# Optimization experiments

Hardware: AMD Instinct MI355X
Metric: run time of the kernel (lower is better)

## Reference

```python
import jax, jax.numpy as jnp
import numpy as np

RPE_LEN = 14  # rpe_length
HEADS = 10
HDIM = 64
EMBED = 640
DFF = 2560


def layer_norm(x, g, b, eps=1e-5):
    mu = jnp.mean(x, axis=-1, keepdims=True)
    var = jnp.var(x, axis=-1, keepdims=True)
    return (x - mu) * jax.lax.rsqrt(var + eps) * g + b


def rpe_embeddings(table_v, table_h, N):
    """RelativePosition2D.forward(N, N) -> [N, N, head_dim]."""
    L = N - 1
    s = int(L ** 0.5)  # 14 for N=197
    r = jnp.arange(L)
    dist_v = r[None, :] // s - r[:, None] // s
    dist_h = r[None, :] % s - r[:, None] % s
    idx_v = jnp.clip(dist_v, -RPE_LEN, RPE_LEN) + RPE_LEN + 1
    idx_h = jnp.clip(dist_h, -RPE_LEN, RPE_LEN) + RPE_LEN + 1
    # pad one row/col of zeros at the front (class token -> index 0)
    idx_v = jnp.pad(idx_v, ((1, 0), (1, 0)))
    idx_h = jnp.pad(idx_h, ((1, 0), (1, 0)))
    return table_v[idx_v] + table_h[idx_h]


def setup_inputs() -> dict:
    key = jax.random.key(0)
    ks = jax.random.split(key, 20)
    B, N, E, H, D, F = 64, 197, EMBED, HEADS, HDIM, DFF
    T = 2 * RPE_LEN + 2  # 30
    std = 0.02
    return {
        "x": jax.random.normal(ks[0], (B, N, E), jnp.float32),
        "ln1_g": jnp.ones((E,), jnp.float32),
        "ln1_b": jnp.zeros((E,), jnp.float32),
        "Wq": jax.random.normal(ks[1], (H * D, E), jnp.float32) * std,
        "Wk": jax.random.normal(ks[2], (H * D, E), jnp.float32) * std,
        "Wv": jax.random.normal(ks[3], (H * D, E), jnp.float32) * std,
        "Wp": jax.random.normal(ks[4], (E, H * D), jnp.float32) * std,
        "bp": jnp.zeros((E,), jnp.float32),
        "rpk_v": jax.random.normal(ks[5], (T, D), jnp.float32) * std,
        "rpk_h": jax.random.normal(ks[6], (T, D), jnp.float32) * std,
        "rpv_v": jax.random.normal(ks[7], (T, D), jnp.float32) * std,
        "rpv_h": jax.random.normal(ks[8], (T, D), jnp.float32) * std,
        "ln2_g": jnp.ones((E,), jnp.float32),
        "ln2_b": jnp.zeros((E,), jnp.float32),
        "W1": jax.random.normal(ks[9], (F, E), jnp.float32) * std,
        "b1": jnp.zeros((F,), jnp.float32),
        "W2": jax.random.normal(ks[10], (E, F), jnp.float32) * std,
        "b2": jnp.zeros((E,), jnp.float32),
    }


def reference(x, ln1_g, ln1_b, Wq, Wk, Wv, Wp, bp,
              rpk_v, rpk_h, rpv_v, rpv_h,
              ln2_g, ln2_b, W1, b1, W2, b2):
    B, N, E = x.shape
    H, D = HEADS, HDIM
    scale = D ** (-0.5)

    # --- attention block (pre-norm) ---
    residual = x
    h = layer_norm(x, ln1_g, ln1_b)
    q = (h @ Wq.T).reshape(B, N, H, D)
    k = (h @ Wk.T).reshape(B, N, H, D)
    v = (h @ Wv.T).reshape(B, N, H, D)

    attn = jnp.einsum('bnhd,bmhd->bhnm', q, k) * scale
    r_p_k = rpe_embeddings(rpk_v, rpk_h, N)          # [N, N, D]
    attn = attn + jnp.einsum('bnhd,nmd->bhnm', q, r_p_k) * scale
    attn = jax.nn.softmax(attn, axis=-1)

    o = jnp.einsum('bhnm,bmhd->bhnd', attn, v)
    r_p_v = rpe_embeddings(rpv_v, rpv_h, N)          # [N, N, D]
    o = o + jnp.einsum('bhnm,nmd->bhnd', attn, r_p_v)
    o = o.transpose(0, 2, 1, 3).reshape(B, N, H * D)
    x = residual + o @ Wp.T + bp

    # --- FFN block (pre-norm) ---
    residual = x
    h = layer_norm(x, ln2_g, ln2_b)
    h = jax.nn.gelu(h @ W1.T + b1, approximate=False)
    x = residual + h @ W2.T + b2
    return x
```

## Files before the change

### kernel.cpp

```cpp
#include <hip/hip_runtime.h>
#include <hip/hip_bf16.h>
#include <math.h>

#define NN   197
#define EE   640
#define HH   10
#define DD   64
#define FF   2560
#define MTOK (64 * 197)
#define RPE_T 30
#define NCONV 17

typedef __hip_bfloat16 bf16;
typedef __attribute__((ext_vector_type(8))) __bf16 bf16x8;
typedef __attribute__((ext_vector_type(4))) float  floatx4;
typedef __attribute__((ext_vector_type(8))) unsigned short ushort8;

#define MFMA32(a, b, c) __builtin_amdgcn_mfma_f32_16x16x32_bf16(a, b, c, 0, 0, 0)

__device__ __forceinline__ float bfbits2f(unsigned short u) {
    union { unsigned int i; float f; } x; x.i = ((unsigned int)u) << 16; return x.f;
}
__device__ __forceinline__ unsigned short f2bf(float f) {
    bf16 t = __float2bfloat16(f);
    unsigned short u; __builtin_memcpy(&u, &t, 2); return u;
}
__device__ __forceinline__ void gld16(const bf16* g, bf16* l) {
    __builtin_amdgcn_global_load_lds(
        (const __attribute__((address_space(1))) unsigned int*)g,
        (__attribute__((address_space(3))) unsigned int*)l, 16, 0, 0);
}
__device__ __forceinline__ float gelu_f(float v) {
    float y = 0.7978845608f * (v + 0.044715f * v * v * v);
    float a = fabsf(y);
    float e = __expf(-2.f * a);
    float t = (1.f - e) / (1.f + e);
    t = (y < 0.f) ? -t : t;
    return 0.5f * v * (1.f + t);
}

__global__ void detect_kernel(const unsigned int* __restrict__ g, int* __restrict__ flag) {
    if (threadIdx.x == 0) flag[0] = (g[0] == 0x3F800000u) ? 1 : 0;
}

struct ConvDesc {
    const void* src[NCONV];
    bf16*       dst[NCONV];
    int         end8[NCONV];
};

__global__ __launch_bounds__(256) void conv_fused(
    ConvDesc d, int total8, const int* __restrict__ flag)
{
    int c = blockIdx.x * 256 + threadIdx.x;
    if (c >= total8) return;
    int s = 0, start = 0;
#pragma unroll
    for (int i = 0; i < NCONV - 1; ++i) {
        if (c >= d.end8[i]) { s = i + 1; start = d.end8[i]; }
    }
    int local = c - start;
    if (flag[0]) {
        const float* sp = (const float*)d.src[s] + (size_t)local * 8;
        bf16 t[8];
#pragma unroll
        for (int j = 0; j < 8; ++j) t[j] = __float2bfloat16(sp[j]);
        *(ushort8*)(d.dst[s] + (size_t)local * 8) = *(const ushort8*)t;
    } else {
        ((ushort8*)d.dst[s])[local] = ((const ushort8*)d.src[s])[local];
    }
}

__global__ __launch_bounds__(256) void rpetrans_kernel(
    const bf16* __restrict__ rvv, const bf16* __restrict__ rvh,
    unsigned short* __restrict__ rvvT, unsigned short* __restrict__ rvhT)
{
    int t = blockIdx.x * 256 + threadIdx.x;
    if (t < 64 * 32) {
        int d = t >> 5, tt = t & 31;
        rvvT[t] = (tt < RPE_T) ? ((const unsigned short*)rvv)[tt * 64 + d] : 0;
        rvhT[t] = (tt < RPE_T) ? ((const unsigned short*)rvh)[tt * 64 + d] : 0;
    }
}

__global__ __launch_bounds__(256) void selbuild_kernel(
    bf16* __restrict__ SelV, bf16* __restrict__ SelH)
{
    int t = blockIdx.x * 256 + threadIdx.x;
    if (t < 16 * 224) {
        int j = t / 224, m = t % 224;
        bool valid = (j < 14) && (m >= 1) && (m < 197);
        SelV[t] = __float2bfloat16((valid && (m - 1) / 14 == j) ? 1.f : 0.f);
        SelH[t] = __float2bfloat16((valid && (m - 1) % 14 == j) ? 1.f : 0.f);
    }
}

__global__ __launch_bounds__(256) void vtrans_kernel(
    const bf16* __restrict__ qkv, unsigned short* __restrict__ VtG)
{
    int bh = blockIdx.x;
    int b = bh / HH, h = bh % HH;
    unsigned short* dst = VtG + (size_t)bh * (64 * 224);
    for (int t = threadIdx.x; t < 224 * 8; t += 256) {
        int m = t >> 3, d8 = (t & 7) << 3;
        ushort8 val = {0, 0, 0, 0, 0, 0, 0, 0};
        if (m < NN)
            val = *(const ushort8*)(qkv + ((size_t)b * NN + m) * 1920 + 1280 + h * 64 + d8);
#pragma unroll
        for (int j = 0; j < 8; ++j) dst[(d8 + j) * 224 + m] = val[j];
    }
}

__global__ __launch_bounds__(256) void ln_kernel(
    const void* __restrict__ xb, size_t xrow0, int xdyn,
    const int* __restrict__ flag,
    const bf16* __restrict__ g, const bf16* __restrict__ b,
    bf16* __restrict__ out, int nrows)
{
    int row  = blockIdx.x * 4 + (threadIdx.x >> 6);
    if (row >= nrows) return;
    int lane = threadIdx.x & 63;
    const int f32 = xdyn && flag[0];
    const size_t base = (xrow0 + row) * (size_t)EE;
    float vals[10];
    float s = 0.f, ss = 0.f;
#pragma unroll
    for (int j = 0; j < 10; ++j) {
        int e = j * 64 + lane;
        float f = f32 ? ((const float*)xb)[base + e]
                      : (float)((const bf16*)xb)[base + e];
        vals[j] = f; s += f; ss += f * f;
    }
#pragma unroll
    for (int off = 32; off; off >>= 1) {
        s  += __shfl_xor(s, off);
        ss += __shfl_xor(ss, off);
    }
    float mean = s * (1.f / EE);
    float var  = ss * (1.f / EE) - mean * mean;
    float rs   = rsqrtf(var + 1e-5f);
#pragma unroll
    for (int j = 0; j < 10; ++j) {
        int e = j * 64 + lane;
        float hv = (vals[j] - mean) * rs * (float)g[e] + (float)b[e];
        out[(size_t)row * EE + e] = __float2bfloat16(hv);
    }
}

template <int KK, int GELU>
__global__ __launch_bounds__(256) void gemm128(
    const bf16* __restrict__ A, const bf16* __restrict__ B,
    const bf16* __restrict__ bias,
    const void* __restrict__ residb, size_t resid_row0, int resid_dyn,
    void* __restrict__ outb, size_t out_row0, int out_dyn,
    const int* __restrict__ flag,
    int M, int N)
{
    __shared__ bf16 At[2][128 * 32];
    __shared__ bf16 Bt[2][128 * 32];

    const int tid  = threadIdx.x;
    const int wave = tid >> 6, lane = tid & 63;
    const int quad = lane >> 4, l16 = lane & 15;
    const int wy = wave >> 1, wx = wave & 1;
    const int n0 = blockIdx.x * 128;
    const int m0 = blockIdx.y * 128;

    const int drow   = wave * 16 + (lane >> 2);
    const int gchunk = ((lane & 3) ^ ((lane >> 3) & 3)) * 8;
    const int ar0 = min(m0 + drow, M - 1);
    const int ar1 = min(m0 + 64 + drow, M - 1);
    const bf16* Ag0 = A + (size_t)ar0 * KK + gchunk;
    const bf16* Ag1 = A + (size_t)ar1 * KK + gchunk;
    const bf16* Bg0 = B + (size_t)(n0 + drow) * KK + gchunk;
    const bf16* Bg1 = B + (size_t)(n0 + 64 + drow) * KK + gchunk;
    const int lo0 = wave * 512;
    const int lo1 = 2048 + wave * 512;

    const int swz = (quad ^ ((l16 >> 1) & 3)) * 8;

    floatx4 acc[4][4] = {};
    constexpr int NK = KK / 64;

    auto body = [&](int k0) {
        __syncthreads();
        gld16(Ag0 + k0,      &At[0][lo0]);
        gld16(Ag1 + k0,      &At[0][lo1]);
        gld16(Ag0 + k0 + 32, &At[1][lo0]);
        gld16(Ag1 + k0 + 32, &At[1][lo1]);
        gld16(Bg0 + k0,      &Bt[0][lo0]);
        gld16(Bg1 + k0,      &Bt[0][lo1]);
        gld16(Bg0 + k0 + 32, &Bt[1][lo0]);
        gld16(Bg1 + k0 + 32, &Bt[1][lo1]);
        __syncthreads();
#pragma unroll
        for (int kk = 0; kk < 2; ++kk) {
            bf16x8 af[4], bfr[4];
#pragma unroll
            for (int s = 0; s < 4; ++s)
                af[s] = *(const bf16x8*)(&At[kk][(wy * 64 + s * 16 + l16) * 32 + swz]);
#pragma unroll
            for (int t = 0; t < 4; ++t)
                bfr[t] = *(const bf16x8*)(&Bt[kk][(wx * 64 + t * 16 + l16) * 32 + swz]);
#pragma unroll
            for (int s = 0; s < 4; ++s)
#pragma unroll
                for (int t = 0; t < 4; ++t)
                    acc[s][t] = MFMA32(af[s], bfr[t], acc[s][t]);
        }
    };

    if constexpr (NK <= 16) {
#pragma unroll
        for (int k = 0; k < NK; ++k) body(k * 64);
    } else {
#pragma unroll 4
        for (int k = 0; k < NK; ++k) body(k * 64);
    }

    const int fr = resid_dyn && flag[0];
    const int fo = out_dyn && flag[0];
    float bv[4];
#pragma unroll
    for (int t = 0; t < 4; ++t)
        bv[t] = bias ? (float)bias[n0 + wx * 64 + t * 16 + l16] : 0.f;

#pragma unroll
    for (int s = 0; s < 4; ++s) {
#pragma unroll
        for (int i = 0; i < 4; ++i) {
            int m = m0 + wy * 64 + s * 16 + quad * 4 + i;
            if (m < M) {
                size_t rowoff_o = (out_row0 + m) * (size_t)N;
                size_t rowoff_r = (resid_row0 + m) * (size_t)N;
#pragma unroll
                for (int t = 0; t < 4; ++t) {
                    int n = n0 + wx * 64 + t * 16 + l16;
                    float v = acc[s][t][i] + bv[t];
                    if (GELU) v = gelu_f(v);
                    if (residb)
                        v += fr ? ((const float*)residb)[rowoff_r + n]
                                : (float)((const bf16*)residb)[rowoff_r + n];
                    if (fo) ((float*)outb)[rowoff_o + n] = v;
                    else    ((bf16*)outb)[rowoff_o + n]  = __float2bfloat16(v);
                }
            }
        }
    }
}

__global__ __launch_bounds__(256) void attn_kernel(
    const bf16* __restrict__ qkv,
    const bf16* __restrict__ tkv, const bf16* __restrict__ tkh,
    const unsigned short* __restrict__ rvvT,
    const unsigned short* __restrict__ rvhT,
    const unsigned short* __restrict__ VtG,
    const bf16* __restrict__ SelV, const bf16* __restrict__ SelH,
    bf16* __restrict__ o)
{
    __shared__ unsigned short Pm[64 * 232];
    __shared__ unsigned short PSv[64 * 40];
    __shared__ unsigned short PSh[64 * 40];
    __shared__ unsigned short QTv[64 * 32];
    __shared__ unsigned short QTh[64 * 32];

    const int tid  = threadIdx.x;
    const int wave = tid >> 6, lane = tid & 63;
    const int quad = lane >> 4, l16 = lane & 15;
    const int b  = blockIdx.x / HH, h = blockIdx.x % HH;
    const int qt = blockIdx.y;
    const size_t rowbase = (size_t)b * NN;

    for (int t = tid; t < 64 * 40; t += 256) { PSv[t] = 0; PSh[t] = 0; }
    for (int t = tid; t < 64 * 24; t += 256) Pm[(t / 24) * 232 + 208 + (t % 24)] = 0;
    __syncthreads();

    const int rA = qt * 64 + wave * 16 + l16;
    const bf16* qrow = qkv + (rowbase + min(rA, NN - 1)) * 1920 + h * 64;
    bf16x8 qa0 = *(const bf16x8*)(qrow + quad * 8);
    bf16x8 qa1 = *(const bf16x8*)(qrow + 32 + quad * 8);

    {
        floatx4 av[2] = {}, ah[2] = {};
#pragma unroll
        for (int ct = 0; ct < 2; ++ct) {
            int t = min(ct * 16 + l16, RPE_T - 1);
            av[ct] = MFMA32(qa0, *(const bf16x8*)(tkv + t * 64 + quad * 8), av[ct]);
            av[ct] = MFMA32(qa1, *(const bf16x8*)(tkv + t * 64 + 32 + quad * 8), av[ct]);
            ah[ct] = MFMA32(qa0, *(const bf16x8*)(tkh + t * 64 + quad * 8), ah[ct]);
            ah[ct] = MFMA32(qa1, *(const bf16x8*)(tkh + t * 64 + 32 + quad * 8), ah[ct]);
        }
#pragma unroll
        for (int ct = 0; ct < 2; ++ct)
#pragma unroll
            for (int i = 0; i < 4; ++i) {
                int row = wave * 16 + quad * 4 + i;
                QTv[row * 32 + ct * 16 + l16] = f2bf(av[ct][i]);
                QTh[row * 32 + ct * 16 + l16] = f2bf(ah[ct][i]);
            }
    }

    floatx4 sacc[13];
#pragma unroll
    for (int mt = 0; mt < 13; ++mt) {
        const bf16* krow = qkv + (rowbase + min(mt * 16 + l16, NN - 1)) * 1920
                           + 640 + h * 64;
        floatx4 a = {};
        a = MFMA32(qa0, *(const bf16x8*)(krow + quad * 8), a);
        a = MFMA32(qa1, *(const bf16x8*)(krow + 32 + quad * 8), a);
        sacc[mt] = a;
    }

    int nn4[4], jn4[4], in4[4];
#pragma unroll
    for (int i = 0; i < 4; ++i) {
        int n = qt * 64 + wave * 16 + quad * 4 + i;
        nn4[i] = n;
        jn4[i] = (n > 0) ? (n - 1) / 14 : 0;
        in4[i] = (n > 0) ? (n - 1) % 14 : 0;
    }
    float mx4[4] = {-3e38f, -3e38f, -3e38f, -3e38f};
#pragma unroll
    for (int mt = 0; mt < 13; ++mt) {
        int m = mt * 16 + l16;
        int jm = (m > 0) ? (m - 1) / 14 : 0;
        int im = (m > 0) ? (m - 1) % 14 : 0;
        bool mok = (m < NN);
#pragma unroll
        for (int i = 0; i < 4; ++i) {
            int row = wave * 16 + quad * 4 + i;
            int iv = (nn4[i] == 0 || m == 0) ? 0 : (jm - jn4[i] + 15);
            int ih = (nn4[i] == 0 || m == 0) ? 0 : (im - in4[i] + 15);
            float val = mok ? (sacc[mt][i] + bfbits2f(QTv[row * 32 + iv])
                               + bfbits2f(QTh[row * 32 + ih])) * 0.125f
                            : -3e38f;
            sacc[mt][i] = val;
            mx4[i] = fmaxf(mx4[i], val);
        }
    }
#pragma unroll
    for (int i = 0; i < 4; ++i)
#pragma unroll
        for (int off = 1; off < 16; off <<= 1)
            mx4[i] = fmaxf(mx4[i], __shfl_xor(mx4[i], off));

    float sm4[4] = {0.f, 0.f, 0.f, 0.f};
#pragma unroll
    for (int mt = 0; mt < 13; ++mt) {
#pragma unroll
        for (int i = 0; i < 4; ++i) {
            float p = __expf(sacc[mt][i] - mx4[i]);
            sm4[i] += p;
            Pm[(wave * 16 + quad * 4 + i) * 232 + mt * 16 + l16] = f2bf(p);
        }
    }
#pragma unroll
    for (int i = 0; i < 4; ++i)
#pragma unroll
        for (int off = 1; off < 16; off <<= 1)
            sm4[i] += __shfl_xor(sm4[i], off);

    floatx4 oacc[4] = {};
    floatx4 psv = {}, psh = {};
    const unsigned short* vt = VtG + (size_t)blockIdx.x * (64 * 224);
    for (int k0 = 0; k0 < 224; k0 += 32) {
        bf16x8 pa = *(const bf16x8*)(const void*)&Pm[(wave * 16 + l16) * 232 + k0 + quad * 8];
#pragma unroll
        for (int ct = 0; ct < 4; ++ct) {
            bf16x8 vb = *(const bf16x8*)(const void*)&vt[(ct * 16 + l16) * 224 + k0 + quad * 8];
            oacc[ct] = MFMA32(pa, vb, oacc[ct]);
        }
        psv = MFMA32(pa, *(const bf16x8*)(SelV + l16 * 224 + k0 + quad * 8), psv);
        psh = MFMA32(pa, *(const bf16x8*)(SelH + l16 * 224 + k0 + quad * 8), psh);
    }

#pragma unroll
    for (int i = 0; i < 4; ++i) {
        int row = wave * 16 + quad * 4 + i;
        int n = qt * 64 + row;
        if (n >= 1 && n < NN && l16 < 14) {
            int jn2 = (n - 1) / 14, in2 = (n - 1) % 14;
            PSv[row * 40 + (l16 - jn2 + 15)] = f2bf(psv[i]);
            PSh[row * 40 + (l16 - in2 + 15)] = f2bf(psh[i]);
        }
    }
    if (lane < 16) {
        int row = wave * 16 + lane;
        int n = qt * 64 + row;
        if (n < NN) {
            float p0 = (n == 0) ? sm4[0] : bfbits2f(Pm[row * 232]);
            PSv[row * 40] = f2bf(p0);
            PSh[row * 40] = f2bf(p0);
        }
    }

    {
        bf16x8 pav = *(const bf16x8*)(const void*)&PSv[(wave * 16 + l16) * 40 + quad * 8];
        bf16x8 pah = *(const bf16x8*)(const void*)&PSh[(wave * 16 + l16) * 40 + quad * 8];
#pragma unroll
        for (int ct = 0; ct < 4; ++ct) {
            bf16x8 bv  = *(const bf16x8*)(const void*)&rvvT[(ct * 16 + l16) * 32 + quad * 8];
            bf16x8 bh2 = *(const bf16x8*)(const void*)&rvhT[(ct * 16 + l16) * 32 + quad * 8];
            oacc[ct] = MFMA32(pav, bv,  oacc[ct]);
            oacc[ct] = MFMA32(pah, bh2, oacc[ct]);
        }
    }
#pragma unroll
    for (int i = 0; i < 4; ++i) {
        float rinv = 1.f / sm4[i];
        int row = wave * 16 + quad * 4 + i;
        int n = qt * 64 + row;
        if (n < NN) {
#pragma unroll
            for (int ct = 0; ct < 4; ++ct)
                o[(rowbase + n) * 640 + h * 64 + ct * 16 + l16] =
                    __float2bfloat16(oacc[ct][i] * rinv);
        }
    }
}

extern "C" void kernel_launch(void* const* d_in, const int* in_sizes, int n_in,
                              void* d_out, int out_size, void* d_ws, size_t ws_size,
                              hipStream_t stream)
{
    const void* xraw = d_in[0];
    char* ws = (char*)d_ws;
    size_t off = 0;
    auto alloc = [&](size_t bytes) -> void* {
        void* p = ws + off;
        off += (bytes + 255) & ~(size_t)255;
        return p;
    };

    int* flag = (int*)alloc(256);
    bf16* Wqc  = (bf16*)alloc((size_t)EE * EE * 2);
    bf16* Wkc  = (bf16*)alloc((size_t)EE * EE * 2);
    bf16* Wvc  = (bf16*)alloc((size_t)EE * EE * 2);
    bf16* Wpc  = (bf16*)alloc((size_t)EE * EE * 2);
    bf16* W1c  = (bf16*)alloc((size_t)FF * EE * 2);
    bf16* W2c  = (bf16*)alloc((size_t)EE * FF * 2);
    bf16* l1g  = (bf16*)alloc(EE * 2);
    bf16* l1b  = (bf16*)alloc(EE * 2);
    bf16* l2g  = (bf16*)alloc(EE * 2);
    bf16* l2b  = (bf16*)alloc(EE * 2);
    bf16* bpc  = (bf16*)alloc(EE * 2);
    bf16* b1c  = (bf16*)alloc(FF * 2);
    bf16* b2c  = (bf16*)alloc(EE * 2);
    bf16* rkv  = (bf16*)alloc(RPE_T * DD * 2);
    bf16* rkh  = (bf16*)alloc(RPE_T * DD * 2);
    bf16* rvv  = (bf16*)alloc(RPE_T * DD * 2);
    bf16* rvh  = (bf16*)alloc(RPE_T * DD * 2);
    unsigned short* rvvT = (unsigned short*)alloc(64 * 32 * 2);
    unsigned short* rvhT = (unsigned short*)alloc(64 * 32 * 2);
    bf16* SelV = (bf16*)alloc(16 * 224 * 2);
    bf16* SelH = (bf16*)alloc(16 * 224 * 2);
    const size_t cvt_end = off;

    int Bc = 0;
    const int cands[6] = {64, 32, 16, 8, 4, 2};
    for (int i = 0; i < 6; ++i) {
        size_t rows = (size_t)NN * cands[i];
        size_t need = cvt_end + rows * 10240 + (size_t)cands[i] * HH * 64 * 224 * 2 + 8192;
        if (need <= ws_size) { Bc = cands[i]; break; }
    }
    if (Bc == 0) return;

    const int nchunks = 64 / Bc;
    const int rows    = NN * Bc;
    bf16* h1   = (bf16*)alloc((size_t)rows * EE * 2);
    bf16* qkvb = (bf16*)alloc((size_t)rows * 1920 * 2);
    bf16* h3   = (bf16*)alloc((size_t)rows * FF * 2);
    unsigned short* VtG = (unsigned short*)alloc((size_t)Bc * HH * 64 * 224 * 2);

    detect_kernel<<<1, 64, 0, stream>>>((const unsigned int*)d_in[1], flag);
    {
        ConvDesc cd;
        const void* srcs[NCONV] = { d_in[3], d_in[4], d_in[5], d_in[6],
                                    d_in[14], d_in[16], d_in[1], d_in[2], d_in[12],
                                    d_in[13], d_in[7], d_in[15], d_in[17], d_in[8],
                                    d_in[9], d_in[10], d_in[11] };
        bf16* dsts[NCONV] = { Wqc, Wkc, Wvc, Wpc, W1c, W2c, l1g, l1b, l2g,
                              l2b, bpc, b1c, b2c, rkv, rkh, rvv, rvh };
        int ns[NCONV] = { EE * EE, EE * EE, EE * EE, EE * EE, FF * EE,
                          EE * FF, EE, EE, EE, EE, EE, FF, EE,
                          RPE_T * DD, RPE_T * DD, RPE_T * DD, RPE_T * DD };
        int cum = 0;
        for (int i = 0; i < NCONV; ++i) {
            cd.src[i] = srcs[i]; cd.dst[i] = dsts[i];
            cum += ns[i] / 8; cd.end8[i] = cum;
        }
        conv_fused<<<(cum + 255) / 256, 256, 0, stream>>>(cd, cum, flag);
    }
    rpetrans_kernel<<<8, 256, 0, stream>>>(rvv, rvh, rvvT, rvhT);
    selbuild_kernel<<<14, 256, 0, stream>>>(SelV, SelH);

    const int gM128 = (rows + 127) / 128;
    const int gLN   = (rows + 3) / 4;

    for (int c = 0; c < nchunks; ++c) {
        const size_t row0 = (size_t)c * rows;

        ln_kernel<<<gLN, 256, 0, stream>>>(xraw, row0, 1, flag, l1g, l1b, h1, rows);

        gemm128<EE, 0><<<dim3(1920 / 128, gM128), 256, 0, stream>>>(
            h1, Wqc, nullptr, nullptr, 0, 0, qkvb, 0, 0, flag, rows, 1920);

        vtrans_kernel<<<Bc * HH, 256, 0, stream>>>(qkvb, VtG);

        attn_kernel<<<dim3(Bc * HH, 4), 256, 0, stream>>>(
            qkvb, rkv, rkh, rvvT, rvhT, VtG, SelV, SelH, h1);

        gemm128<EE, 0><<<dim3(EE / 128, gM128), 256, 0, stream>>>(
            h1, Wpc, bpc, xraw, row0, 1, d_out, row0, 1, flag, rows, EE);
    }

    for (int c = 0; c < nchunks; ++c) {
        const size_t row0 = (size_t)c * rows;

        ln_kernel<<<gLN, 256, 0, stream>>>(d_out, row0, 1, flag, l2g, l2b, h1, rows);

        gemm128<EE, 1><<<dim3(FF / 128, gM128), 256, 0, stream>>>(
            h1, W1c, b1c, nullptr, 0, 0, h3, 0, 0, flag, rows, FF);

        gemm128<FF, 0><<<dim3(EE / 128, gM128), 256, 0, stream>>>(
            h3, W2c, b2c, d_out, row0, 1, d_out, row0, 1, flag, rows, EE);
    }
}
```

Before: 479.2 us.

## Pre-swizzle K, V, RPE tables and selectors into MFMA fragment order

Adds a pre-pass that rewrites K, V, the RPE key/value tables and the selector matrices into a lane-contiguous MFMA operand layout. The attention kernel can then fetch each B fragment as one contiguous 16-byte load per lane instead of strided row gathers. K is now copied as well as V, which adds extra global traffic in the transpose kernel, and the V transpose does scalar strided reads. The intent is better coalescing in the attention inner loops.

```diff
diff --git a/kernel.cpp b/kernel.cpp
--- a/kernel.cpp
+++ b/kernel.cpp
@@ -71,43 +71,61 @@
     }
 }
 
-__global__ __launch_bounds__(256) void rpetrans_kernel(
+__global__ __launch_bounds__(256) void tabflat_kernel(
+    const bf16* __restrict__ tkv, const bf16* __restrict__ tkh,
     const bf16* __restrict__ rvv, const bf16* __restrict__ rvh,
-    unsigned short* __restrict__ rvvT, unsigned short* __restrict__ rvhT)
-{
-    int t = blockIdx.x * 256 + threadIdx.x;
-    if (t < 64 * 32) {
-        int d = t >> 5, tt = t & 31;
-        rvvT[t] = (tt < RPE_T) ? ((const unsigned short*)rvv)[tt * 64 + d] : 0;
-        rvhT[t] = (tt < RPE_T) ? ((const unsigned short*)rvh)[tt * 64 + d] : 0;
-    }
-}
-
-__global__ __launch_bounds__(256) void selbuild_kernel(
-    bf16* __restrict__ SelV, bf16* __restrict__ SelH)
-{
-    int t = blockIdx.x * 256 + threadIdx.x;
-    if (t < 16 * 224) {
-        int j = t / 224, m = t % 224;
-        bool valid = (j < 14) && (m >= 1) && (m < 197);
-        SelV[t] = __float2bfloat16((valid && (m - 1) / 14 == j) ? 1.f : 0.f);
-        SelH[t] = __float2bfloat16((valid && (m - 1) % 14 == j) ? 1.f : 0.f);
-    }
-}
-
-__global__ __launch_bounds__(256) void vtrans_kernel(
-    const bf16* __restrict__ qkv, unsigned short* __restrict__ VtG)
+    unsigned short* __restrict__ tkvL, unsigned short* __restrict__ tkhL,
+    unsigned short* __restrict__ rvvL, unsigned short* __restrict__ rvhL,
+    bf16* __restrict__ SelVL, bf16* __restrict__ SelHL)
+{
+    int i = blockIdx.x * 256 + threadIdx.x;
+    int f = i >> 9, r = i & 511, quad = r >> 7, l16 = (r >> 3) & 15, j = i & 7;
+    if (i < 2048) {
+        int ct = f >> 1, kk = f & 1, t = ct * 16 + l16, d = kk * 32 + quad * 8 + j;
+        tkvL[i] = (t < RPE_T) ? ((const unsigned short*)tkv)[t * 64 + d] : 0;
+        tkhL[i] = (t < RPE_T) ? ((const unsigned short*)tkh)[t * 64 + d] : 0;
+        int d2 = f * 16 + l16, t2 = quad * 8 + j;
+        rvvL[i] = (t2 < RPE_T) ? ((const unsigned short*)rvv)[t2 * 64 + d2] : 0;
+        rvhL[i] = (t2 < RPE_T) ? ((const unsigned short*)rvh)[t2 * 64 + d2] : 0;
+    }
+    if (i < 3584) {
+        int m = f * 32 + quad * 8 + j;
+        bool ok = (l16 < 14) && (m >= 1) && (m < NN);
+        SelVL[i] = __float2bfloat16((ok && (m - 1) / 14 == l16) ? 1.f : 0.f);
+        SelHL[i] = __float2bfloat16((ok && (m - 1) % 14 == l16) ? 1.f : 0.f);
+    }
+}
+
+__global__ __launch_bounds__(256) void kvtrans_kernel(
+    const bf16* __restrict__ qkv,
+    unsigned short* __restrict__ KtL, unsigned short* __restrict__ VtL)
 {
     int bh = blockIdx.x;
     int b = bh / HH, h = bh % HH;
-    unsigned short* dst = VtG + (size_t)bh * (64 * 224);
-    for (int t = threadIdx.x; t < 224 * 8; t += 256) {
-        int m = t >> 3, d8 = (t & 7) << 3;
+    unsigned short* kd = KtL + (size_t)bh * (26 * 512);
+    unsigned short* vd = VtL + (size_t)bh * (28 * 512);
+    for (int o = threadIdx.x; o < 26 * 64; o += 256) {
+        int f = o >> 6, lane = o & 63, quad = lane >> 4, l16 = lane & 15;
+        int mt = f >> 1, kk = f & 1;
+        int m = mt * 16 + l16, d = kk * 32 + quad * 8;
         ushort8 val = {0, 0, 0, 0, 0, 0, 0, 0};
         if (m < NN)
-            val = *(const ushort8*)(qkv + ((size_t)b * NN + m) * 1920 + 1280 + h * 64 + d8);
-#pragma unroll
-        for (int j = 0; j < 8; ++j) dst[(d8 + j) * 224 + m] = val[j];
+            val = *(const ushort8*)(qkv + ((size_t)b * NN + m) * 1920 + 640 + h * 64 + d);
+        *(ushort8*)(kd + o * 8) = val;
+    }
+    for (int o = threadIdx.x; o < 28 * 64; o += 256) {
+        int f = o >> 6, lane = o & 63, quad = lane >> 4, l16 = lane & 15;
+        int kc = f >> 2, ct = f & 3;
+        int d = ct * 16 + l16, mbase = kc * 32 + quad * 8;
+        unsigned short val[8];
+#pragma unroll
+        for (int j = 0; j < 8; ++j) {
+            int m = mbase + j;
+            val[j] = (m < NN)
+                ? ((const unsigned short*)qkv)[((size_t)b * NN + m) * 1920 + 1280 + h * 64 + d]
+                : 0;
+        }
+        *(ushort8*)(vd + o * 8) = *(const ushort8*)val;
     }
 }
 
@@ -251,11 +269,11 @@
 
 __global__ __launch_bounds__(256) void attn_kernel(
     const bf16* __restrict__ qkv,
-    const bf16* __restrict__ tkv, const bf16* __restrict__ tkh,
-    const unsigned short* __restrict__ rvvT,
-    const unsigned short* __restrict__ rvhT,
-    const unsigned short* __restrict__ VtG,
-    const bf16* __restrict__ SelV, const bf16* __restrict__ SelH,
+    const unsigned short* __restrict__ tkvL, const unsigned short* __restrict__ tkhL,
+    const unsigned short* __restrict__ rvvL, const unsigned short* __restrict__ rvhL,
+    const unsigned short* __restrict__ KtL,
+    const unsigned short* __restrict__ VtL,
+    const bf16* __restrict__ SelVL, const bf16* __restrict__ SelHL,
     bf16* __restrict__ o)
 {
     __shared__ unsigned short Pm[64 * 232];
@@ -270,6 +288,9 @@
     const int b  = blockIdx.x / HH, h = blockIdx.x % HH;
     const int qt = blockIdx.y;
     const size_t rowbase = (size_t)b * NN;
+    const unsigned short* kt = KtL + (size_t)blockIdx.x * (26 * 512);
+    const unsigned short* vt = VtL + (size_t)blockIdx.x * (28 * 512);
+    const int le8 = lane * 8;
 
     for (int t = tid; t < 64 * 40; t += 256) { PSv[t] = 0; PSh[t] = 0; }
     for (int t = tid; t < 64 * 24; t += 256) Pm[(t / 24) * 232 + 208 + (t % 24)] = 0;
@@ -284,11 +305,10 @@
         floatx4 av[2] = {}, ah[2] = {};
 #pragma unroll
         for (int ct = 0; ct < 2; ++ct) {
-            int t = min(ct * 16 + l16, RPE_T - 1);
-            av[ct] = MFMA32(qa0, *(const bf16x8*)(tkv + t * 64 + quad * 8), av[ct]);
-            av[ct] = MFMA32(qa1, *(const bf16x8*)(tkv + t * 64 + 32 + quad * 8), av[ct]);
-            ah[ct] = MFMA32(qa0, *(const bf16x8*)(tkh + t * 64 + quad * 8), ah[ct]);
-            ah[ct] = MFMA32(qa1, *(const bf16x8*)(tkh + t * 64 + 32 + quad * 8), ah[ct]);
+            av[ct] = MFMA32(qa0, *(const bf16x8*)(const void*)&tkvL[(ct * 2 + 0) * 512 + le8], av[ct]);
+            av[ct] = MFMA32(qa1, *(const bf16x8*)(const void*)&tkvL[(ct * 2 + 1) * 512 + le8], av[ct]);
+            ah[ct] = MFMA32(qa0, *(const bf16x8*)(const void*)&tkhL[(ct * 2 + 0) * 512 + le8], ah[ct]);
+            ah[ct] = MFMA32(qa1, *(const bf16x8*)(const void*)&tkhL[(ct * 2 + 1) * 512 + le8], ah[ct]);
         }
 #pragma unroll
         for (int ct = 0; ct < 2; ++ct)
@@ -303,11 +323,9 @@
     floatx4 sacc[13];
 #pragma unroll
     for (int mt = 0; mt < 13; ++mt) {
-        const bf16* krow = qkv + (rowbase + min(mt * 16 + l16, NN - 1)) * 1920
-                           + 640 + h * 64;
         floatx4 a = {};
-        a = MFMA32(qa0, *(const bf16x8*)(krow + quad * 8), a);
-        a = MFMA32(qa1, *(const bf16x8*)(krow + 32 + quad * 8), a);
+        a = MFMA32(qa0, *(const bf16x8*)(const void*)&kt[(mt * 2 + 0) * 512 + le8], a);
+        a = MFMA32(qa1, *(const bf16x8*)(const void*)&kt[(mt * 2 + 1) * 512 + le8], a);
         sacc[mt] = a;
     }
 
@@ -362,16 +380,16 @@
 
     floatx4 oacc[4] = {};
     floatx4 psv = {}, psh = {};
-    const unsigned short* vt = VtG + (size_t)blockIdx.x * (64 * 224);
-    for (int k0 = 0; k0 < 224; k0 += 32) {
-        bf16x8 pa = *(const bf16x8*)(const void*)&Pm[(wave * 16 + l16) * 232 + k0 + quad * 8];
+#pragma unroll
+    for (int kc = 0; kc < 7; ++kc) {
+        bf16x8 pa = *(const bf16x8*)(const void*)&Pm[(wave * 16 + l16) * 232 + kc * 32 + quad * 8];
 #pragma unroll
         for (int ct = 0; ct < 4; ++ct) {
-            bf16x8 vb = *(const bf16x8*)(const void*)&vt[(ct * 16 + l16) * 224 + k0 + quad * 8];
+            bf16x8 vb = *(const bf16x8*)(const void*)&vt[(kc * 4 + ct) * 512 + le8];
             oacc[ct] = MFMA32(pa, vb, oacc[ct]);
         }
-        psv = MFMA32(pa, *(const bf16x8*)(SelV + l16 * 224 + k0 + quad * 8), psv);
-        psh = MFMA32(pa, *(const bf16x8*)(SelH + l16 * 224 + k0 + quad * 8), psh);
+        psv = MFMA32(pa, *(const bf16x8*)(SelVL + kc * 512 + le8), psv);
+        psh = MFMA32(pa, *(const bf16x8*)(SelHL + kc * 512 + le8), psh);
     }
 
 #pragma unroll
@@ -399,8 +417,8 @@
         bf16x8 pah = *(const bf16x8*)(const void*)&PSh[(wave * 16 + l16) * 40 + quad * 8];
 #pragma unroll
         for (int ct = 0; ct < 4; ++ct) {
-            bf16x8 bv  = *(const bf16x8*)(const void*)&rvvT[(ct * 16 + l16) * 32 + quad * 8];
-            bf16x8 bh2 = *(const bf16x8*)(const void*)&rvhT[(ct * 16 + l16) * 32 + quad * 8];
+            bf16x8 bv  = *(const bf16x8*)(const void*)&rvvL[ct * 512 + le8];
+            bf16x8 bh2 = *(const bf16x8*)(const void*)&rvhL[ct * 512 + le8];
             oacc[ct] = MFMA32(pav, bv,  oacc[ct]);
             oacc[ct] = MFMA32(pah, bh2, oacc[ct]);
         }
@@ -450,17 +468,20 @@
     bf16* rkh  = (bf16*)alloc(RPE_T * DD * 2);
     bf16* rvv  = (bf16*)alloc(RPE_T * DD * 2);
     bf16* rvh  = (bf16*)alloc(RPE_T * DD * 2);
-    unsigned short* rvvT = (unsigned short*)alloc(64 * 32 * 2);
-    unsigned short* rvhT = (unsigned short*)alloc(64 * 32 * 2);
-    bf16* SelV = (bf16*)alloc(16 * 224 * 2);
-    bf16* SelH = (bf16*)alloc(16 * 224 * 2);
+    unsigned short* tkvL = (unsigned short*)alloc(2048 * 2);
+    unsigned short* tkhL = (unsigned short*)alloc(2048 * 2);
+    unsigned short* rvvL = (unsigned short*)alloc(2048 * 2);
+    unsigned short* rvhL = (unsigned short*)alloc(2048 * 2);
+    bf16* SelVL = (bf16*)alloc(3584 * 2);
+    bf16* SelHL = (bf16*)alloc(3584 * 2);
     const size_t cvt_end = off;
 
     int Bc = 0;
     const int cands[6] = {64, 32, 16, 8, 4, 2};
     for (int i = 0; i < 6; ++i) {
         size_t rows = (size_t)NN * cands[i];
-        size_t need = cvt_end + rows * 10240 + (size_t)cands[i] * HH * 64 * 224 * 2 + 8192;
+        size_t need = cvt_end + rows * 10240
+                      + (size_t)cands[i] * HH * (26 + 28) * 512 * 2 + 8192;
         if (need <= ws_size) { Bc = cands[i]; break; }
     }
     if (Bc == 0) return;
@@ -470,7 +491,8 @@
     bf16* h1   = (bf16*)alloc((size_t)rows * EE * 2);
     bf16* qkvb = (bf16*)alloc((size_t)rows * 1920 * 2);
     bf16* h3   = (bf16*)alloc((size_t)rows * FF * 2);
-    unsigned short* VtG = (unsigned short*)alloc((size_t)Bc * HH * 64 * 224 * 2);
+    unsigned short* KtL = (unsigned short*)alloc((size_t)Bc * HH * 26 * 512 * 2);
+    unsigned short* VtL = (unsigned short*)alloc((size_t)Bc * HH * 28 * 512 * 2);
 
     detect_kernel<<<1, 64, 0, stream>>>((const unsigned int*)d_in[1], flag);
     {
@@ -491,8 +513,8 @@
         }
         conv_fused<<<(cum + 255) / 256, 256, 0, stream>>>(cd, cum, flag);
     }
-    rpetrans_kernel<<<8, 256, 0, stream>>>(rvv, rvh, rvvT, rvhT);
-    selbuild_kernel<<<14, 256, 0, stream>>>(SelV, SelH);
+    tabflat_kernel<<<14, 256, 0, stream>>>(rkv, rkh, rvv, rvh,
+                                           tkvL, tkhL, rvvL, rvhL, SelVL, SelHL);
 
     const int gM128 = (rows + 127) / 128;
     const int gLN   = (rows + 3) / 4;
@@ -505,10 +527,10 @@
         gemm128<EE, 0><<<dim3(1920 / 128, gM128), 256, 0, stream>>>(
             h1, Wqc, nullptr, nullptr, 0, 0, qkvb, 0, 0, flag, rows, 1920);
 
-        vtrans_kernel<<<Bc * HH, 256, 0, stream>>>(qkvb, VtG);
+        kvtrans_kernel<<<Bc * HH, 256, 0, stream>>>(qkvb, KtL, VtL);
 
         attn_kernel<<<dim3(Bc * HH, 4), 256, 0, stream>>>(
-            qkvb, rkv, rkh, rvvT, rvhT, VtG, SelV, SelH, h1);
+            qkvb, tkvL, tkhL, rvvL, rvhL, KtL, VtL, SelVL, SelHL, h1);
 
         gemm128<EE, 0><<<dim3(EE / 128, gM128), 256, 0, stream>>>(
             h1, Wpc, bpc, xraw, row0, 1, d_out, row0, 1, flag, rows, EE);
```

New measurement: 446.0 us. 6.9% less time.
